# Optimization experiments

Measured on AMD Instinct MI355X. Metric: run time of the kernel, lower is better.

The kernel has to match this reference:

```python
import jax, jax.numpy as jnp
import numpy as np
from jax import lax

B, C, H, W = 8, 256, 32, 32
HEADS = 8
NUM_OFF = 9
OFF_SCALE = 0.1


def setup_inputs() -> dict:
    key = jax.random.key(0)
    ks = jax.random.split(key, 8)
    f = lambda k, s, sc: jax.random.normal(k, s, dtype=jnp.float32) * sc
    return {
        'query_map': f(ks[0], (B, C, H, W), 1.0),
        'kv_map': f(ks[1], (B, C, H, W), 1.0),
        'Wq': f(ks[2], (C, C), C ** -0.5),
        'Wk': f(ks[3], (C, C), C ** -0.5),
        'Wv': f(ks[4], (C, C), C ** -0.5),
        'Woff1': f(ks[5], (C // 2, C, 3, 3), (C * 9) ** -0.5),
        'boff1': jnp.zeros((C // 2,), jnp.float32),
        'Woff2': f(ks[6], (NUM_OFF * 2, C // 2), (C // 2) ** -0.5),
        'boff2': jnp.zeros((NUM_OFF * 2,), jnp.float32),
        'Wout': f(ks[7], (C, C), C ** -0.5),
        'bout': jnp.zeros((C,), jnp.float32),
    }


def grid_sample_bilinear_border(img, grid):
    """img: (B,C,H,W); grid: (B,H,W,2) with (x,y) in [-1,1], align_corners=True,
    padding_mode='border'. Returns (B,C,H,W)."""
    Bn, Cn, Hn, Wn = img.shape
    x = (grid[..., 0] + 1.0) * 0.5 * (Wn - 1)
    y = (grid[..., 1] + 1.0) * 0.5 * (Hn - 1)
    # border padding: clamp continuous coords into the valid range
    x = jnp.clip(x, 0.0, Wn - 1)
    y = jnp.clip(y, 0.0, Hn - 1)
    x0 = jnp.floor(x)
    y0 = jnp.floor(y)
    wx = x - x0
    wy = y - y0
    x0i = x0.astype(jnp.int32)
    y0i = y0.astype(jnp.int32)
    x1i = jnp.minimum(x0i + 1, Wn - 1)
    y1i = jnp.minimum(y0i + 1, Hn - 1)
    flat = img.reshape(Bn, Cn, Hn * Wn)

    def gat(iy, ix):
        idx = (iy * Wn + ix).reshape(Bn, 1, -1)  # broadcasts over channels
        return jnp.take_along_axis(flat, idx, axis=2)

    v00 = gat(y0i, x0i)
    v01 = gat(y0i, x1i)
    v10 = gat(y1i, x0i)
    v11 = gat(y1i, x1i)
    wxf = wx.reshape(Bn, 1, -1)
    wyf = wy.reshape(Bn, 1, -1)
    out = (v00 * (1 - wxf) + v01 * wxf) * (1 - wyf) + (v10 * (1 - wxf) + v11 * wxf) * wyf
    return out.reshape(Bn, Cn, Hn, Wn)


def reference(query_map, kv_map, Wq, Wk, Wv, Woff1, boff1, Woff2, boff2, Wout, bout):
    Bn, Cn, Hn, Wn = query_map.shape
    hd = Cn // HEADS
    # 1x1 conv projections as channel einsums
    q = jnp.einsum('oc,bchw->bohw', Wq, query_map)
    # offset network: 3x3 conv -> relu -> 1x1 conv
    h1 = lax.conv_general_dilated(q, Woff1, (1, 1), 'SAME',
                                  dimension_numbers=('NCHW', 'OIHW', 'NCHW'))
    h1 = jax.nn.relu(h1 + boff1[None, :, None, None])
    offsets = jnp.einsum('oc,bchw->bohw', Woff2, h1) + boff2[None, :, None, None]
    offsets = offsets.reshape(Bn, NUM_OFF, 2, Hn, Wn)
    offset = offsets[:, 0] * OFF_SCALE  # (B,2,H,W); ch0 -> x, ch1 -> y
    # normalized base grid in [-1,1] (align_corners=True convention)
    gx = jnp.linspace(-1.0, 1.0, Wn, dtype=q.dtype)[None, :]  # (1,W)
    gy = jnp.linspace(-1.0, 1.0, Hn, dtype=q.dtype)[:, None]  # (H,1)
    vx = gx[None] + offset[:, 0]  # (B,H,W)
    vy = gy[None] + offset[:, 1]
    vgrid = jnp.stack([vx, vy], axis=-1)  # (B,H,W,2)
    kv_sampled = grid_sample_bilinear_border(kv_map, vgrid)
    k = jnp.einsum('oc,bchw->bohw', Wk, kv_sampled)
    v = jnp.einsum('oc,bchw->bohw', Wv, kv_sampled)
    # (B,C,H,W) -> (B,heads,HW,hd)
    def to_heads(t):
        return t.reshape(Bn, HEADS, hd, Hn * Wn).transpose(0, 1, 3, 2)
    qh, kh, vh = to_heads(q), to_heads(k), to_heads(v)
    scale = hd ** -0.5
    attn = jnp.einsum('bhqd,bhkd->bhqk', qh, kh) * scale
    attn = jax.nn.softmax(attn, axis=-1)
    out = jnp.einsum('bhqk,bhkd->bhqd', attn, vh)
    out = out.transpose(0, 1, 3, 2).reshape(Bn, Cn, Hn, Wn)
    out = jnp.einsum('oc,bchw->bohw', Wout, out) + bout[None, :, None, None]
    return out
```

## Files before the change

kernel.cpp:

```cpp
#include <hip/hip_runtime.h>

#define HW_ 1024

typedef __attribute__((ext_vector_type(8))) short bf16x8;
typedef __attribute__((ext_vector_type(4))) short bf16x4;
typedef __attribute__((ext_vector_type(4))) float f32x4;

__device__ inline unsigned short f2bf(float f) {
  unsigned int u = __float_as_uint(f);
  u += 0x7FFF + ((u >> 16) & 1);
  return (unsigned short)(u >> 16);
}
__device__ inline unsigned short f2bf_fast(float f) {
  return (unsigned short)((__float_as_uint(f) + 0x8000u) >> 16);
}
__device__ inline float bf2f(unsigned short h) {
  return __uint_as_float(((unsigned int)h) << 16);
}
__device__ inline void async_copy16(const void* g, void* l) {
  __builtin_amdgcn_global_load_lds(
      (const __attribute__((address_space(1))) unsigned int*)g,
      (__attribute__((address_space(3))) unsigned int*)l, 16, 0, 0);
}

__global__ __launch_bounds__(256) void prep(
    const float* __restrict__ kv,
    const float* __restrict__ Wq, const float* __restrict__ Wk,
    const float* __restrict__ Wv, const float* __restrict__ Wo,
    const float* __restrict__ Woff1,
    short* __restrict__ WH, short* __restrict__ WL, short* __restrict__ wb,
    float* __restrict__ kvT)
{
  __shared__ float T[256][33];
  const int bid = blockIdx.x, t = threadIdx.x;

  if (bid < 256) {
    int b = bid >> 5, p0 = (bid & 31) * 32;
    int pp = t & 31, cg = t >> 5;
#pragma unroll
    for (int i = 0; i < 32; ++i) {
      int c = cg * 32 + i;
      T[c][pp] = kv[((size_t)(b * 256 + c)) * HW_ + p0 + pp];
    }
    __syncthreads();
#pragma unroll
    for (int r = 0; r < 8; ++r) {
      int e = t + 256 * r;
      int c4 = (e & 63) * 4, pp2 = e >> 6;
      float4 v4;
      v4.x = T[c4 + 0][pp2];
      v4.y = T[c4 + 1][pp2];
      v4.z = T[c4 + 2][pp2];
      v4.w = T[c4 + 3][pp2];
      *(float4*)&kvT[((size_t)(b * 1024 + p0 + pp2)) * 256 + c4] = v4;
    }
  } else if (bid < 512) {
    int b2 = bid - 256;
    int mat = b2 >> 6;
    int loc = (b2 & 63) * 1024 + t * 4;
    const float* W = (mat == 0) ? Wq : (mat == 1) ? Wk : (mat == 2) ? Wv : Wo;
    float4 f4 = *(const float4*)&W[loc];
    float f[4] = {f4.x, f4.y, f4.z, f4.w};
    bf16x4 h4, l4;
#pragma unroll
    for (int j = 0; j < 4; ++j) {
      unsigned short h = f2bf(f[j]);
      h4[j] = (short)h;
      l4[j] = (short)f2bf(f[j] - bf2f(h));
    }
    int r = loc >> 8, c = loc & 255;
    int mtile = r >> 4, k0s = c >> 5;
    int lane_ = ((c >> 3) & 3) * 16 + (r & 15);
    int pidx = (((mtile * 8 + k0s) * 64 + lane_) * 8) + (c & 7);
    *(bf16x4*)&WH[mat * 65536 + pidx] = h4;
    *(bf16x4*)&WL[mat * 65536 + pidx] = l4;
  } else {
    int e0 = (bid - 512) * 1024 + t * 4;
    int c = e0 & 255;
    int o = (e0 >> 8) & 127;
    int tap = e0 >> 15;
    bf16x4 h4;
#pragma unroll
    for (int j = 0; j < 4; ++j)
      h4[j] = (short)f2bf(Woff1[((size_t)(o * 256 + c + j)) * 9 + tap]);
    int otile = o >> 4, c0s = c >> 5;
    int lane_ = ((c >> 3) & 3) * 16 + (o & 15);
    int widx = ((((tap * 8 + otile) * 8 + c0s) * 64 + lane_) * 8) + (c & 7);
    *(bf16x4*)&wb[widx] = h4;
  }
}

__global__ __launch_bounds__(512) void qgemm(
    const short* __restrict__ WH, const short* __restrict__ WL,
    const float* __restrict__ Xf,
    short* __restrict__ Yt, short* __restrict__ Yh2, short* __restrict__ Yl2)
{
  __shared__ short Bsh[32][264];
  __shared__ short Bsl[32][264];
  const int t    = threadIdx.x;
  const int w    = t >> 6;
  const int lane = t & 63;
  const int ln   = lane & 15;
  const int qd   = lane >> 4;
  const int bp0  = blockIdx.x * 32;
  const int bB   = bp0 >> 10, p0l = bp0 & 1023;

  {
    int pp = t & 31, cs = t >> 5;
    float fv[16];
#pragma unroll
    for (int j = 0; j < 16; ++j)
      fv[j] = Xf[((size_t)(bB * 256 + cs * 16 + j)) * HW_ + p0l + pp];
#pragma unroll
    for (int g = 0; g < 4; ++g) {
      bf16x4 h4, l4;
#pragma unroll
      for (int j = 0; j < 4; ++j) {
        float f = fv[g * 4 + j];
        unsigned short h = f2bf(f);
        h4[j] = (short)h;
        l4[j] = (short)f2bf(f - bf2f(h));
      }
      *(bf16x4*)&Bsh[pp][cs * 16 + g * 4] = h4;
      *(bf16x4*)&Bsl[pp][cs * 16 + g * 4] = l4;
    }
  }
  __syncthreads();

  const int mh = w >> 2, ww = w & 3;
  const int mb = mh * 8 + ww * 2;
  f32x4 acc[2][2] = {};
#pragma unroll
  for (int k0 = 0; k0 < 256; k0 += 32) {
    const int k0s = k0 >> 5;
    bf16x8 Ah[2], Al[2], Bh[2], Bl[2];
#pragma unroll
    for (int mt = 0; mt < 2; ++mt) {
      size_t wi = ((size_t)(((mb + mt) * 8 + k0s) * 64 + lane)) * 8;
      Ah[mt] = *(const bf16x8*)&WH[wi];
      Al[mt] = *(const bf16x8*)&WL[wi];
    }
#pragma unroll
    for (int nt = 0; nt < 2; ++nt) {
      Bh[nt] = *(const bf16x8*)&Bsh[nt * 16 + ln][k0 + qd * 8];
      Bl[nt] = *(const bf16x8*)&Bsl[nt * 16 + ln][k0 + qd * 8];
    }
#pragma unroll
    for (int mt = 0; mt < 2; ++mt)
#pragma unroll
      for (int nt = 0; nt < 2; ++nt) {
        acc[mt][nt] = __builtin_amdgcn_mfma_f32_16x16x32_bf16(Ah[mt], Bh[nt], acc[mt][nt], 0, 0, 0);
        acc[mt][nt] = __builtin_amdgcn_mfma_f32_16x16x32_bf16(Ah[mt], Bl[nt], acc[mt][nt], 0, 0, 0);
        acc[mt][nt] = __builtin_amdgcn_mfma_f32_16x16x32_bf16(Al[mt], Bh[nt], acc[mt][nt], 0, 0, 0);
      }
  }

  const int om = mh * 128 + ww * 32;
  const float sc = 0.25506063286f;
#pragma unroll
  for (int mt = 0; mt < 2; ++mt)
#pragma unroll
    for (int nt = 0; nt < 2; ++nt) {
      int bp = bp0 + nt * 16 + ln;
      int b = bp >> 10, p = bp & 1023;
#pragma unroll
      for (int i = 0; i < 4; ++i) {
        int o = om + mt * 16 + qd * 4 + i;
        int h = o >> 5, d = o & 31;
        Yt[(((size_t)(b * 8 + h)) * 1024 + p) * 32 + d] = (short)f2bf(acc[mt][nt][i] * sc);
      }
      int ob = om + mt * 16 + qd * 4;
      bf16x4 h4, l4;
#pragma unroll
      for (int i = 0; i < 4; ++i) {
        float f = acc[mt][nt][i];
        unsigned short h = f2bf(f);
        h4[i] = (short)h;
        l4[i] = (short)f2bf(f - bf2f(h));
      }
      *(bf16x4*)&Yh2[(size_t)bp * 256 + ob] = h4;
      *(bf16x4*)&Yl2[(size_t)bp * 256 + ob] = l4;
    }
}

__global__ __launch_bounds__(512) void convkv(
    const short* __restrict__ wb, const float* __restrict__ bias,
    const float* __restrict__ W2, const float* __restrict__ b2,
    const short* __restrict__ xh, const short* __restrict__ xl,
    const float* __restrict__ kvT,
    const short* __restrict__ WH, const short* __restrict__ WL,
    short* __restrict__ kt, short* __restrict__ vt)
{
  __shared__ short Xs[2][3][34][264];
  __shared__ short XsH[32][264];
  __shared__ short XsL[32][264];
  __shared__ float red[4][32][2];
  __shared__ float2 crd[32];
  const int id   = blockIdx.x;
  const int b    = id & 7;
  const int y0   = id >> 3;
  const int t    = threadIdx.x;
  const int w    = t >> 6;
  const int lane = t & 63;
  const int ln   = lane & 15;
  const int qd   = lane >> 4;
  const int bp0  = (b * 32 + y0) * 32;

  {
    bf16x8 v[12];
#pragma unroll
    for (int i = 0; i < 12; ++i) {
      int e = t + 512 * i;
      int oct = e & 31;
      int x   = (e >> 5) & 31;
      int rr  = e >> 10;
      int hl  = rr / 3, r = rr % 3;
      int yy  = y0 + r - 1;
      bf16x8 val = {};
      if (yy >= 0 && yy < 32) {
        const short* src = hl ? xl : xh;
        val = *(const bf16x8*)&src[((size_t)((b * 32 + yy) * 32 + x)) * 256 + oct * 8];
      }
      v[i] = val;
    }
#pragma unroll
    for (int i = 0; i < 12; ++i) {
      int e = t + 512 * i;
      int oct = e & 31;
      int x   = (e >> 5) & 31;
      int rr  = e >> 10;
      int hl  = rr / 3, r = rr % 3;
      *(bf16x8*)&Xs[hl][r][x + 1][oct * 8] = v[i];
    }
    if (t < 384) {
      int oct  = t & 31;
      int colw = (t >> 5) & 1;
      int rr   = t >> 6;
      int hl   = rr / 3, r = rr % 3;
      bf16x8 zz = {};
      *(bf16x8*)&Xs[hl][r][colw ? 33 : 0][oct * 8] = zz;
    }
  }
  __syncthreads();

  const int chh = w >> 2;
  const int ow  = w & 3;
  const int o0c = ow * 32;
  f32x4 acc[2][2] = {};
#pragma unroll
  for (int c0s = 0; c0s < 4; ++c0s) {
    const int c0 = chh * 128 + c0s * 32;
    const int c0abs = chh * 4 + c0s;
#pragma unroll
    for (int tap = 0; tap < 9; ++tap) {
      const int ky = tap / 3, kx = tap % 3;
      bf16x8 afr[2];
#pragma unroll
      for (int m = 0; m < 2; ++m)
        afr[m] = *(const bf16x8*)&wb[((((tap * 8 + (ow * 2 + m)) * 8 + c0abs) * 64
                                       + lane) * 8)];
#pragma unroll
      for (int nt = 0; nt < 2; ++nt) {
        int hc = nt * 16 + ln + kx;
        bf16x8 bh = *(const bf16x8*)&Xs[0][ky][hc][c0 + qd * 8];
        bf16x8 bl = *(const bf16x8*)&Xs[1][ky][hc][c0 + qd * 8];
#pragma unroll
        for (int m = 0; m < 2; ++m) {
          acc[m][nt] = __builtin_amdgcn_mfma_f32_16x16x32_bf16(afr[m], bh, acc[m][nt], 0, 0, 0);
          acc[m][nt] = __builtin_amdgcn_mfma_f32_16x16x32_bf16(afr[m], bl, acc[m][nt], 0, 0, 0);
        }
      }
    }
  }

  float* ps = (float*)&XsH[0][0];
  if (w >= 4) {
#pragma unroll
    for (int m = 0; m < 2; ++m)
#pragma unroll
      for (int nt = 0; nt < 2; ++nt)
        *(f32x4*)&ps[(((w - 4) * 64 + lane) * 4 + m * 2 + nt) * 4] = acc[m][nt];
  }
  __syncthreads();

  if (w < 4) {
    float ps0[2] = {0.f, 0.f}, ps1[2] = {0.f, 0.f};
#pragma unroll
    for (int m = 0; m < 2; ++m)
#pragma unroll
      for (int nt = 0; nt < 2; ++nt) {
        f32x4 p = *(const f32x4*)&ps[((w * 64 + lane) * 4 + m * 2 + nt) * 4];
        acc[m][nt] += p;
      }
#pragma unroll
    for (int m = 0; m < 2; ++m)
#pragma unroll
      for (int i = 0; i < 4; ++i) {
        int o = o0c + m * 16 + qd * 4 + i;
        float bo = bias[o];
        float w2a = W2[o], w2b = W2[128 + o];
#pragma unroll
        for (int nt = 0; nt < 2; ++nt) {
          float h = fmaxf(acc[m][nt][i] + bo, 0.f);
          ps0[nt] += w2a * h;
          ps1[nt] += w2b * h;
        }
      }
#pragma unroll
    for (int msk = 16; msk < 64; msk <<= 1) {
      ps0[0] += __shfl_xor(ps0[0], msk, 64);
      ps0[1] += __shfl_xor(ps0[1], msk, 64);
      ps1[0] += __shfl_xor(ps1[0], msk, 64);
      ps1[1] += __shfl_xor(ps1[1], msk, 64);
    }
    if (qd == 0) {
#pragma unroll
      for (int nt = 0; nt < 2; ++nt) {
        red[w][nt * 16 + ln][0] = ps0[nt];
        red[w][nt * 16 + ln][1] = ps1[nt];
      }
    }
  }
  __syncthreads();
  if (t < 32) {
    float c0s = (red[0][t][0] + red[1][t][0]) + (red[2][t][0] + red[3][t][0]) + b2[0];
    float c1s = (red[0][t][1] + red[1][t][1]) + (red[2][t][1] + red[3][t][1]) + b2[1];
    float gx = -1.f + 2.f * (float)t / 31.f;
    float gy = -1.f + 2.f * (float)y0 / 31.f;
    float vx = gx + 0.1f * c0s;
    float vy = gy + 0.1f * c1s;
    float px = fminf(fmaxf((vx + 1.f) * 0.5f * 31.f, 0.f), 31.f);
    float py = fminf(fmaxf((vy + 1.f) * 0.5f * 31.f, 0.f), 31.f);
    crd[t] = make_float2(px, py);
  }
  __syncthreads();

#pragma unroll
  for (int it = 0; it < 2; ++it) {
    int e = t + 512 * it;
    int oct = e & 31, row = e >> 5;
    float2 cd = crd[row];
    float x0f = floorf(cd.x), y0f = floorf(cd.y);
    float wx = cd.x - x0f, wy = cd.y - y0f;
    int x0 = (int)x0f, y0i = (int)y0f;
    int x1 = min(x0 + 1, 31), y1 = min(y0i + 1, 31);
    float w00 = (1.f - wx) * (1.f - wy), w01 = wx * (1.f - wy);
    float w10 = (1.f - wx) * wy,         w11 = wx * wy;
    const float* r00 = &kvT[((size_t)(b * 1024 + y0i * 32 + x0)) * 256 + oct * 8];
    const float* r01 = &kvT[((size_t)(b * 1024 + y0i * 32 + x1)) * 256 + oct * 8];
    const float* r10 = &kvT[((size_t)(b * 1024 + y1 * 32 + x0)) * 256 + oct * 8];
    const float* r11 = &kvT[((size_t)(b * 1024 + y1 * 32 + x1)) * 256 + oct * 8];
    float4 a00 = *(const float4*)r00, b00 = *(const float4*)(r00 + 4);
    float4 a01 = *(const float4*)r01, b01 = *(const float4*)(r01 + 4);
    float4 a10 = *(const float4*)r10, b10 = *(const float4*)(r10 + 4);
    float4 a11 = *(const float4*)r11, b11 = *(const float4*)(r11 + 4);
    float v[8];
    v[0] = a00.x * w00 + a01.x * w01 + a10.x * w10 + a11.x * w11;
    v[1] = a00.y * w00 + a01.y * w01 + a10.y * w10 + a11.y * w11;
    v[2] = a00.z * w00 + a01.z * w01 + a10.z * w10 + a11.z * w11;
    v[3] = a00.w * w00 + a01.w * w01 + a10.w * w10 + a11.w * w11;
    v[4] = b00.x * w00 + b01.x * w01 + b10.x * w10 + b11.x * w11;
    v[5] = b00.y * w00 + b01.y * w01 + b10.y * w10 + b11.y * w11;
    v[6] = b00.z * w00 + b01.z * w01 + b10.z * w10 + b11.z * w11;
    v[7] = b00.w * w00 + b01.w * w01 + b10.w * w10 + b11.w * w11;
    bf16x8 h8, l8;
#pragma unroll
    for (int j = 0; j < 8; ++j) {
      unsigned short h = f2bf(v[j]);
      h8[j] = (short)h;
      l8[j] = (short)f2bf(v[j] - bf2f(h));
    }
    *(bf16x8*)&XsH[row][oct * 8] = h8;
    *(bf16x8*)&XsL[row][oct * 8] = l8;
  }
  __syncthreads();

  const int mat  = w >> 2;
  const short* WAh = WH + (mat ? 131072 : 65536);
  const short* WAl = WL + (mat ? 131072 : 65536);
  const int om4 = (w & 3) * 4;

  f32x4 acg[4][2] = {};
#pragma unroll
  for (int k0 = 0; k0 < 256; k0 += 32) {
    const int k0s = k0 >> 5;
    bf16x8 Bh[2], Bl[2];
#pragma unroll
    for (int nt = 0; nt < 2; ++nt) {
      Bh[nt] = *(const bf16x8*)&XsH[nt * 16 + ln][k0 + qd * 8];
      Bl[nt] = *(const bf16x8*)&XsL[nt * 16 + ln][k0 + qd * 8];
    }
#pragma unroll
    for (int mt = 0; mt < 4; ++mt) {
      size_t wi = ((size_t)(((om4 + mt) * 8 + k0s) * 64 + lane)) * 8;
      bf16x8 Ah = *(const bf16x8*)&WAh[wi];
      bf16x8 Al = *(const bf16x8*)&WAl[wi];
#pragma unroll
      for (int nt = 0; nt < 2; ++nt) {
        acg[mt][nt] = __builtin_amdgcn_mfma_f32_16x16x32_bf16(Ah, Bh[nt], acg[mt][nt], 0, 0, 0);
        acg[mt][nt] = __builtin_amdgcn_mfma_f32_16x16x32_bf16(Ah, Bl[nt], acg[mt][nt], 0, 0, 0);
        acg[mt][nt] = __builtin_amdgcn_mfma_f32_16x16x32_bf16(Al, Bh[nt], acg[mt][nt], 0, 0, 0);
      }
    }
  }

#pragma unroll
  for (int mt = 0; mt < 4; ++mt)
#pragma unroll
    for (int nt = 0; nt < 2; ++nt) {
      int p  = bp0 + nt * 16 + ln;
      int pl = p & 1023;
      int jt = pl >> 6, jl = pl & 63;
#pragma unroll
      for (int i = 0; i < 4; ++i) {
        int oc = (w & 3) * 64 + mt * 16 + qd * 4 + i;
        unsigned short val = f2bf(acg[mt][nt][i]);
        int bhead = b * 8 + (oc >> 5), d = oc & 31;
        if (mat == 0) {
          int cd2 = (d >> 3) ^ ((jl >> 2) & 3);
          kt[((((size_t)(bhead * 16 + jt)) * 64 + jl) * 4 + cd2) * 8 + (d & 7)] = (short)val;
        } else {
          int jjs = ((jl & 15) << 2) | (jl >> 4);
          int cj = (jjs >> 3) ^ (d & 7);
          vt[((((size_t)(bhead * 16 + jt)) * 32 + d) * 8 + cj) * 8 + (jjs & 7)] = (short)val;
        }
      }
    }
}

__global__ __launch_bounds__(512) void attn_mfma(
    const short* __restrict__ qt, const short* __restrict__ kt,
    const short* __restrict__ vt, short* __restrict__ aoh,
    short* __restrict__ aol)
{
  __shared__ __align__(16) short Ks[2][2048];
  __shared__ __align__(16) short Vs[2][2048];
  __shared__ __align__(16) short P[8][32][72];
  const int t    = threadIdx.x;
  const int w    = t >> 6;
  const int lane = t & 63;
  const int ln   = lane & 15;
  const int qd   = lane >> 4;
  const int bid  = blockIdx.x;
  const int b    = bid & 7;
  const int rem2 = bid >> 3;
  const int h    = rem2 & 7;
  const int qp   = rem2 >> 3;
  const int bh   = b * 8 + h;
  const int qce  = qp + 4 * (w >> 2);
  const int qbase = qce * 128 + (w & 3) * 16;

  const short* ktb = kt + (size_t)bh * 32768;
  const short* vtb = vt + (size_t)bh * 32768;

  bf16x8 aq[2];
  aq[0] = *(const bf16x8*)&qt[((size_t)(bh * 1024 + qbase + ln)) * 32 + qd * 8];
  aq[1] = *(const bf16x8*)&qt[((size_t)(bh * 1024 + qbase + 64 + ln)) * 32 + qd * 8];

  f32x4 acc[2][2] = {};
  float lacc[2][4] = {};
  const f32x4 zero = {0.f, 0.f, 0.f, 0.f};

  const int sgw   = w & 3;
  const int stoff = sgw * 512 + lane * 8;
  const int ldoff = sgw * 512;

  if (w < 4) async_copy16(&ktb[stoff], &Ks[0][ldoff]);
  else       async_copy16(&vtb[stoff], &Vs[0][ldoff]);
  __syncthreads();

  for (int jt = 0; jt < 16; ++jt) {
    const int cur = jt & 1, nxt = cur ^ 1;
    if (jt < 15) {
      if (w < 4) async_copy16(&ktb[(jt + 1) * 2048 + stoff], &Ks[nxt][ldoff]);
      else       async_copy16(&vtb[(jt + 1) * 2048 + stoff], &Vs[nxt][ldoff]);
    }

    bf16x8 bk[4], bv[2][2];
#pragma unroll
    for (int kk = 0; kk < 4; ++kk)
      bk[kk] = *(const bf16x8*)&Ks[cur][((kk * 16 + ln) * 4 + (qd ^ ((ln >> 2) & 3))) * 8];
#pragma unroll
    for (int kc = 0; kc < 2; ++kc)
#pragma unroll
      for (int ds = 0; ds < 2; ++ds)
        bv[kc][ds] = *(const bf16x8*)&Vs[cur][((ds * 16 + ln) * 8 + ((kc * 4 + qd) ^ (ln & 7))) * 8];

#pragma unroll
    for (int qf = 0; qf < 2; ++qf) {
      f32x4 s[4];
      __builtin_amdgcn_s_setprio(1);
#pragma unroll
      for (int kk = 0; kk < 4; ++kk)
        s[kk] = __builtin_amdgcn_mfma_f32_16x16x32_bf16(aq[qf], bk[kk], zero, 0, 0, 0);
      __builtin_amdgcn_s_setprio(0);

#pragma unroll
      for (int i = 0; i < 4; ++i) {
        float p0 = __builtin_amdgcn_exp2f(s[0][i]);
        float p1 = __builtin_amdgcn_exp2f(s[1][i]);
        float p2 = __builtin_amdgcn_exp2f(s[2][i]);
        float p3 = __builtin_amdgcn_exp2f(s[3][i]);
        s[0][i] = p0; s[1][i] = p1; s[2][i] = p2; s[3][i] = p3;
        lacc[qf][i] += (p0 + p1) + (p2 + p3);
      }
#pragma unroll
      for (int i = 0; i < 4; ++i) {
        bf16x4 p4;
#pragma unroll
        for (int kk = 0; kk < 4; ++kk) p4[kk] = (short)f2bf_fast(s[kk][i]);
        *(bf16x4*)&P[w][qf * 16 + qd * 4 + i][4 * ln] = p4;
      }
      __builtin_amdgcn_s_setprio(1);
#pragma unroll
      for (int kc = 0; kc < 2; ++kc) {
        bf16x8 ap = *(const bf16x8*)&P[w][qf * 16 + ln][kc * 32 + qd * 8];
#pragma unroll
        for (int ds = 0; ds < 2; ++ds)
          acc[qf][ds] = __builtin_amdgcn_mfma_f32_16x16x32_bf16(ap, bv[kc][ds], acc[qf][ds], 0, 0, 0);
      }
      __builtin_amdgcn_s_setprio(0);
    }

    __syncthreads();
  }

  const int bb = bh >> 3, hh2 = bh & 7;
#pragma unroll
  for (int qf = 0; qf < 2; ++qf)
#pragma unroll
    for (int i = 0; i < 4; ++i) {
      float l = lacc[qf][i];
      l += __shfl_xor(l, 1, 64);
      l += __shfl_xor(l, 2, 64);
      l += __shfl_xor(l, 4, 64);
      l += __shfl_xor(l, 8, 64);
      float inv = 1.f / l;
      int qrow = qbase + qf * 64 + qd * 4 + i;
#pragma unroll
      for (int ds = 0; ds < 2; ++ds) {
        float v = acc[qf][ds][i] * inv;
        unsigned short hv = f2bf(v);
        size_t idx = ((size_t)(bb * 1024 + qrow)) * 256 + hh2 * 32 + ds * 16 + ln;
        aoh[idx] = (short)hv;
        aol[idx] = (short)f2bf(v - bf2f(hv));
      }
    }
}

__global__ __launch_bounds__(512) void gemm_out(
    const short* __restrict__ Wh, const short* __restrict__ Wl,
    const short* __restrict__ Xh, const short* __restrict__ Xl,
    const float* __restrict__ bias, float* __restrict__ Yf)
{
  __shared__ short XsH[32][264];
  __shared__ short XsL[32][264];
  const int t    = threadIdx.x;
  const int w    = t >> 6;
  const int lane = t & 63;
  const int ln   = lane & 15;
  const int qd   = lane >> 4;
  const int bp0  = blockIdx.x * 32;

#pragma unroll
  for (int it = 0; it < 2; ++it) {
    int e = t + 512 * it;
    int oct = e & 31, row = e >> 5;
    bf16x8 vh = *(const bf16x8*)&Xh[((size_t)(bp0 + row)) * 256 + oct * 8];
    bf16x8 vl = *(const bf16x8*)&Xl[((size_t)(bp0 + row)) * 256 + oct * 8];
    *(bf16x8*)&XsH[row][oct * 8] = vh;
    *(bf16x8*)&XsL[row][oct * 8] = vl;
  }
  __syncthreads();

  const int mh = w >> 2, ww = w & 3;
  const int mb = mh * 8 + ww * 2;
  f32x4 acc[2][2] = {};
#pragma unroll
  for (int k0 = 0; k0 < 256; k0 += 32) {
    const int k0s = k0 >> 5;
    bf16x8 Ah[2], Al[2], Bh[2], Bl[2];
#pragma unroll
    for (int mt = 0; mt < 2; ++mt) {
      size_t wi = ((size_t)(((mb + mt) * 8 + k0s) * 64 + lane)) * 8;
      Ah[mt] = *(const bf16x8*)&Wh[wi];
      Al[mt] = *(const bf16x8*)&Wl[wi];
    }
#pragma unroll
    for (int nt = 0; nt < 2; ++nt) {
      Bh[nt] = *(const bf16x8*)&XsH[nt * 16 + ln][k0 + qd * 8];
      Bl[nt] = *(const bf16x8*)&XsL[nt * 16 + ln][k0 + qd * 8];
    }
#pragma unroll
    for (int mt = 0; mt < 2; ++mt)
#pragma unroll
      for (int nt = 0; nt < 2; ++nt) {
        acc[mt][nt] = __builtin_amdgcn_mfma_f32_16x16x32_bf16(Ah[mt], Bh[nt], acc[mt][nt], 0, 0, 0);
        acc[mt][nt] = __builtin_amdgcn_mfma_f32_16x16x32_bf16(Ah[mt], Bl[nt], acc[mt][nt], 0, 0, 0);
        acc[mt][nt] = __builtin_amdgcn_mfma_f32_16x16x32_bf16(Al[mt], Bh[nt], acc[mt][nt], 0, 0, 0);
      }
  }

  const int om = mh * 128 + ww * 32;
#pragma unroll
  for (int mt = 0; mt < 2; ++mt)
#pragma unroll
    for (int i = 0; i < 4; ++i) {
      int o = om + mt * 16 + qd * 4 + i;
      float bo = bias[o];
#pragma unroll
      for (int nt = 0; nt < 2; ++nt) {
        int bp = bp0 + nt * 16 + ln;
        int b = bp >> 10, p = bp & 1023;
        Yf[((size_t)(b * 256 + o)) * HW_ + p] = acc[mt][nt][i] + bo;
      }
    }
}

extern "C" void kernel_launch(void* const* d_in, const int* in_sizes, int n_in,
                              void* d_out, int out_size, void* d_ws, size_t ws_size,
                              hipStream_t stream)
{
  const float* query_map = (const float*)d_in[0];
  const float* kv_map    = (const float*)d_in[1];
  const float* Wq        = (const float*)d_in[2];
  const float* Wk        = (const float*)d_in[3];
  const float* Wv        = (const float*)d_in[4];
  const float* Woff1     = (const float*)d_in[5];
  const float* boff1     = (const float*)d_in[6];
  const float* Woff2     = (const float*)d_in[7];
  const float* boff2     = (const float*)d_in[8];
  const float* Wout      = (const float*)d_in[9];
  const float* bout      = (const float*)d_in[10];
  float* out = (float*)d_out;
  char* base = (char*)d_ws;

  const size_t MB = 1u << 20;
  short* qt     = (short*)(base + 1 * MB);
  short* kt     = (short*)(base + 5 * MB);
  short* vt     = (short*)(base + 9 * MB);
  short* bufBh  = (short*)(base + 13 * MB);
  short* bufBl  = (short*)(base + 17 * MB);
  short* wb     = (short*)(base + 21 * MB);
  short* WH     = (short*)(base + 22 * MB);
  short* WL     = (short*)(base + 23 * MB);
  float* kvT    = (float*)(base + 24 * MB);

  prep<<<dim3(800), dim3(256), 0, stream>>>(kv_map, Wq, Wk, Wv, Wout, Woff1,
                                            WH, WL, wb, kvT);
  qgemm<<<dim3(256), dim3(512), 0, stream>>>(WH, WL, query_map,
                                             qt, bufBh, bufBl);
  convkv<<<dim3(256), dim3(512), 0, stream>>>(wb, boff1, Woff2, boff2,
                                              bufBh, bufBl, kvT, WH, WL, kt, vt);
  attn_mfma<<<dim3(256), dim3(512), 0, stream>>>(qt, kt, vt, bufBh, bufBl);
  gemm_out<<<dim3(256), dim3(512), 0, stream>>>(WH + 196608, WL + 196608,
                                                bufBh, bufBl, bout, out);
}
```

Before: 157.5 us.

## Fuse Q projection GEMM with remaining prep work into one launch

```diff
diff --git a/kernel.cpp b/kernel.cpp
--- a/kernel.cpp
+++ b/kernel.cpp
@@ -23,29 +23,143 @@
       (__attribute__((address_space(3))) unsigned int*)l, 16, 0, 0);
 }
 
-__global__ __launch_bounds__(256) void prep(
+__global__ __launch_bounds__(256) void prepQ(
+    const float* __restrict__ Wq,
+    short* __restrict__ WH, short* __restrict__ WL)
+{
+  const int t = threadIdx.x;
+  int loc = blockIdx.x * 1024 + t * 4;
+  float4 f4 = *(const float4*)&Wq[loc];
+  float f[4] = {f4.x, f4.y, f4.z, f4.w};
+  bf16x4 h4, l4;
+#pragma unroll
+  for (int j = 0; j < 4; ++j) {
+    unsigned short h = f2bf(f[j]);
+    h4[j] = (short)h;
+    l4[j] = (short)f2bf(f[j] - bf2f(h));
+  }
+  int r = loc >> 8, c = loc & 255;
+  int mtile = r >> 4, k0s = c >> 5;
+  int lane_ = ((c >> 3) & 3) * 16 + (r & 15);
+  int pidx = (((mtile * 8 + k0s) * 64 + lane_) * 8) + (c & 7);
+  *(bf16x4*)&WH[pidx] = h4;
+  *(bf16x4*)&WL[pidx] = l4;
+}
+
+__global__ __launch_bounds__(512) void fusedQP(
+    const short* __restrict__ WH0, const short* __restrict__ WL0,
+    const float* __restrict__ Xf,
     const float* __restrict__ kv,
-    const float* __restrict__ Wq, const float* __restrict__ Wk,
-    const float* __restrict__ Wv, const float* __restrict__ Wo,
-    const float* __restrict__ Woff1,
+    const float* __restrict__ Wk, const float* __restrict__ Wv,
+    const float* __restrict__ Wo, const float* __restrict__ Woff1,
     short* __restrict__ WH, short* __restrict__ WL, short* __restrict__ wb,
-    float* __restrict__ kvT)
+    float* __restrict__ kvT,
+    short* __restrict__ Yt, short* __restrict__ Yh2, short* __restrict__ Yl2)
 {
+  __shared__ short Bsh[32][264];
+  __shared__ short Bsl[32][264];
   __shared__ float T[256][33];
-  const int bid = blockIdx.x, t = threadIdx.x;
+  const int bid = blockIdx.x;
+  const int t   = threadIdx.x;
 
   if (bid < 256) {
-    int b = bid >> 5, p0 = (bid & 31) * 32;
-    int pp = t & 31, cg = t >> 5;
-#pragma unroll
-    for (int i = 0; i < 32; ++i) {
-      int c = cg * 32 + i;
+    const int w    = t >> 6;
+    const int lane = t & 63;
+    const int ln   = lane & 15;
+    const int qd   = lane >> 4;
+    const int bp0  = bid * 32;
+    const int bB   = bp0 >> 10, p0l = bp0 & 1023;
+
+    {
+      int pp = t & 31, cs = t >> 5;
+      float fv[16];
+#pragma unroll
+      for (int j = 0; j < 16; ++j)
+        fv[j] = Xf[((size_t)(bB * 256 + cs * 16 + j)) * HW_ + p0l + pp];
+#pragma unroll
+      for (int g = 0; g < 4; ++g) {
+        bf16x4 h4, l4;
+#pragma unroll
+        for (int j = 0; j < 4; ++j) {
+          float f = fv[g * 4 + j];
+          unsigned short h = f2bf(f);
+          h4[j] = (short)h;
+          l4[j] = (short)f2bf(f - bf2f(h));
+        }
+        *(bf16x4*)&Bsh[pp][cs * 16 + g * 4] = h4;
+        *(bf16x4*)&Bsl[pp][cs * 16 + g * 4] = l4;
+      }
+    }
+    __syncthreads();
+
+    const int mh = w >> 2, ww = w & 3;
+    const int mb = mh * 8 + ww * 2;
+    f32x4 acc[2][2] = {};
+#pragma unroll
+    for (int k0 = 0; k0 < 256; k0 += 32) {
+      const int k0s = k0 >> 5;
+      bf16x8 Ah[2], Al[2], Bh[2], Bl[2];
+#pragma unroll
+      for (int mt = 0; mt < 2; ++mt) {
+        size_t wi = ((size_t)(((mb + mt) * 8 + k0s) * 64 + lane)) * 8;
+        Ah[mt] = *(const bf16x8*)&WH0[wi];
+        Al[mt] = *(const bf16x8*)&WL0[wi];
+      }
+#pragma unroll
+      for (int nt = 0; nt < 2; ++nt) {
+        Bh[nt] = *(const bf16x8*)&Bsh[nt * 16 + ln][k0 + qd * 8];
+        Bl[nt] = *(const bf16x8*)&Bsl[nt * 16 + ln][k0 + qd * 8];
+      }
+#pragma unroll
+      for (int mt = 0; mt < 2; ++mt)
+#pragma unroll
+        for (int nt = 0; nt < 2; ++nt) {
+          acc[mt][nt] = __builtin_amdgcn_mfma_f32_16x16x32_bf16(Ah[mt], Bh[nt], acc[mt][nt], 0, 0, 0);
+          acc[mt][nt] = __builtin_amdgcn_mfma_f32_16x16x32_bf16(Ah[mt], Bl[nt], acc[mt][nt], 0, 0, 0);
+          acc[mt][nt] = __builtin_amdgcn_mfma_f32_16x16x32_bf16(Al[mt], Bh[nt], acc[mt][nt], 0, 0, 0);
+        }
+    }
+
+    const int om = mh * 128 + ww * 32;
+    const float sc = 0.25506063286f;
+#pragma unroll
+    for (int mt = 0; mt < 2; ++mt)
+#pragma unroll
+      for (int nt = 0; nt < 2; ++nt) {
+        int bp = bp0 + nt * 16 + ln;
+        int b = bp >> 10, p = bp & 1023;
+#pragma unroll
+        for (int i = 0; i < 4; ++i) {
+          int o = om + mt * 16 + qd * 4 + i;
+          int h = o >> 5, d = o & 31;
+          Yt[(((size_t)(b * 8 + h)) * 1024 + p) * 32 + d] = (short)f2bf(acc[mt][nt][i] * sc);
+        }
+        int ob = om + mt * 16 + qd * 4;
+        bf16x4 h4, l4;
+#pragma unroll
+        for (int i = 0; i < 4; ++i) {
+          float f = acc[mt][nt][i];
+          unsigned short h = f2bf(f);
+          h4[i] = (short)h;
+          l4[i] = (short)f2bf(f - bf2f(h));
+        }
+        *(bf16x4*)&Yh2[(size_t)bp * 256 + ob] = h4;
+        *(bf16x4*)&Yl2[(size_t)bp * 256 + ob] = l4;
+      }
+
+  } else if (bid < 512) {
+    int tb = bid - 256;
+    int b = tb >> 5, p0 = (tb & 31) * 32;
+    int pp = t & 31, cg16 = t >> 5;
+#pragma unroll
+    for (int i = 0; i < 16; ++i) {
+      int c = cg16 * 16 + i;
       T[c][pp] = kv[((size_t)(b * 256 + c)) * HW_ + p0 + pp];
     }
     __syncthreads();
 #pragma unroll
-    for (int r = 0; r < 8; ++r) {
-      int e = t + 256 * r;
+    for (int r = 0; r < 4; ++r) {
+      int e = t + 512 * r;
       int c4 = (e & 63) * 4, pp2 = e >> 6;
       float4 v4;
       v4.x = T[c4 + 0][pp2];
@@ -54,11 +168,11 @@
       v4.w = T[c4 + 3][pp2];
       *(float4*)&kvT[((size_t)(b * 1024 + p0 + pp2)) * 256 + c4] = v4;
     }
-  } else if (bid < 512) {
-    int b2 = bid - 256;
-    int mat = b2 >> 6;
-    int loc = (b2 & 63) * 1024 + t * 4;
-    const float* W = (mat == 0) ? Wq : (mat == 1) ? Wk : (mat == 2) ? Wv : Wo;
+  } else if (bid < 608) {
+    int g = (bid - 512) * 2048 + t * 4;
+    int mat = 1 + (g >> 16);
+    int loc = g & 65535;
+    const float* W = (mat == 1) ? Wk : (mat == 2) ? Wv : Wo;
     float4 f4 = *(const float4*)&W[loc];
     float f[4] = {f4.x, f4.y, f4.z, f4.w};
     bf16x4 h4, l4;
@@ -75,7 +189,7 @@
     *(bf16x4*)&WH[mat * 65536 + pidx] = h4;
     *(bf16x4*)&WL[mat * 65536 + pidx] = l4;
   } else {
-    int e0 = (bid - 512) * 1024 + t * 4;
+    int e0 = (bid - 608) * 2048 + t * 4;
     int c = e0 & 255;
     int o = (e0 >> 8) & 127;
     int tap = e0 >> 15;
@@ -88,99 +202,6 @@
     int widx = ((((tap * 8 + otile) * 8 + c0s) * 64 + lane_) * 8) + (c & 7);
     *(bf16x4*)&wb[widx] = h4;
   }
-}
-
-__global__ __launch_bounds__(512) void qgemm(
-    const short* __restrict__ WH, const short* __restrict__ WL,
-    const float* __restrict__ Xf,
-    short* __restrict__ Yt, short* __restrict__ Yh2, short* __restrict__ Yl2)
-{
-  __shared__ short Bsh[32][264];
-  __shared__ short Bsl[32][264];
-  const int t    = threadIdx.x;
-  const int w    = t >> 6;
-  const int lane = t & 63;
-  const int ln   = lane & 15;
-  const int qd   = lane >> 4;
-  const int bp0  = blockIdx.x * 32;
-  const int bB   = bp0 >> 10, p0l = bp0 & 1023;
-
-  {
-    int pp = t & 31, cs = t >> 5;
-    float fv[16];
-#pragma unroll
-    for (int j = 0; j < 16; ++j)
-      fv[j] = Xf[((size_t)(bB * 256 + cs * 16 + j)) * HW_ + p0l + pp];
-#pragma unroll
-    for (int g = 0; g < 4; ++g) {
-      bf16x4 h4, l4;
-#pragma unroll
-      for (int j = 0; j < 4; ++j) {
-        float f = fv[g * 4 + j];
-        unsigned short h = f2bf(f);
-        h4[j] = (short)h;
-        l4[j] = (short)f2bf(f - bf2f(h));
-      }
-      *(bf16x4*)&Bsh[pp][cs * 16 + g * 4] = h4;
-      *(bf16x4*)&Bsl[pp][cs * 16 + g * 4] = l4;
-    }
-  }
-  __syncthreads();
-
-  const int mh = w >> 2, ww = w & 3;
-  const int mb = mh * 8 + ww * 2;
-  f32x4 acc[2][2] = {};
-#pragma unroll
-  for (int k0 = 0; k0 < 256; k0 += 32) {
-    const int k0s = k0 >> 5;
-    bf16x8 Ah[2], Al[2], Bh[2], Bl[2];
-#pragma unroll
-    for (int mt = 0; mt < 2; ++mt) {
-      size_t wi = ((size_t)(((mb + mt) * 8 + k0s) * 64 + lane)) * 8;
-      Ah[mt] = *(const bf16x8*)&WH[wi];
-      Al[mt] = *(const bf16x8*)&WL[wi];
-    }
-#pragma unroll
-    for (int nt = 0; nt < 2; ++nt) {
-      Bh[nt] = *(const bf16x8*)&Bsh[nt * 16 + ln][k0 + qd * 8];
-      Bl[nt] = *(const bf16x8*)&Bsl[nt * 16 + ln][k0 + qd * 8];
-    }
-#pragma unroll
-    for (int mt = 0; mt < 2; ++mt)
-#pragma unroll
-      for (int nt = 0; nt < 2; ++nt) {
-        acc[mt][nt] = __builtin_amdgcn_mfma_f32_16x16x32_bf16(Ah[mt], Bh[nt], acc[mt][nt], 0, 0, 0);
-        acc[mt][nt] = __builtin_amdgcn_mfma_f32_16x16x32_bf16(Ah[mt], Bl[nt], acc[mt][nt], 0, 0, 0);
-        acc[mt][nt] = __builtin_amdgcn_mfma_f32_16x16x32_bf16(Al[mt], Bh[nt], acc[mt][nt], 0, 0, 0);
-      }
-  }
-
-  const int om = mh * 128 + ww * 32;
-  const float sc = 0.25506063286f;
-#pragma unroll
-  for (int mt = 0; mt < 2; ++mt)
-#pragma unroll
-    for (int nt = 0; nt < 2; ++nt) {
-      int bp = bp0 + nt * 16 + ln;
-      int b = bp >> 10, p = bp & 1023;
-#pragma unroll
-      for (int i = 0; i < 4; ++i) {
-        int o = om + mt * 16 + qd * 4 + i;
-        int h = o >> 5, d = o & 31;
-        Yt[(((size_t)(b * 8 + h)) * 1024 + p) * 32 + d] = (short)f2bf(acc[mt][nt][i] * sc);
-      }
-      int ob = om + mt * 16 + qd * 4;
-      bf16x4 h4, l4;
-#pragma unroll
-      for (int i = 0; i < 4; ++i) {
-        float f = acc[mt][nt][i];
-        unsigned short h = f2bf(f);
-        h4[i] = (short)h;
-        l4[i] = (short)f2bf(f - bf2f(h));
-      }
-      *(bf16x4*)&Yh2[(size_t)bp * 256 + ob] = h4;
-      *(bf16x4*)&Yl2[(size_t)bp * 256 + ob] = l4;
-    }
 }
 
 __global__ __launch_bounds__(512) void convkv(
@@ -646,10 +667,11 @@
   short* WL     = (short*)(base + 23 * MB);
   float* kvT    = (float*)(base + 24 * MB);
 
-  prep<<<dim3(800), dim3(256), 0, stream>>>(kv_map, Wq, Wk, Wv, Wout, Woff1,
-                                            WH, WL, wb, kvT);
-  qgemm<<<dim3(256), dim3(512), 0, stream>>>(WH, WL, query_map,
-                                             qt, bufBh, bufBl);
+  prepQ<<<dim3(64), dim3(256), 0, stream>>>(Wq, WH, WL);
+  fusedQP<<<dim3(752), dim3(512), 0, stream>>>(WH, WL, query_map,
+                                               kv_map, Wk, Wv, Wout, Woff1,
+                                               WH, WL, wb, kvT,
+                                               qt, bufBh, bufBl);
   convkv<<<dim3(256), dim3(512), 0, stream>>>(wb, boff1, Woff2, boff2,
                                               bufBh, bufBl, kvT, WH, WL, kt, vt);
   attn_mfma<<<dim3(256), dim3(512), 0, stream>>>(qt, kt, vt, bufBh, bufBl);
```

Measured after the change: 156.2 us. About the same (-0.8%).
